# Kernel tuning notes

Measured on AMD Instinct MI355X. Metric: run time of the kernel, lower is better.

## Reference

```python
import jax, jax.numpy as jnp
import numpy as np

B, T, D, K, NF = 4, 1024, 1024, 4, 4
MAXD = 256          # TemporalEncoding max_delta
NC = 32             # ConceptGraph n_concepts
LN_EPS = 1e-5


def setup_inputs() -> dict:
    key = jax.random.key(0)
    ks = jax.random.split(key, 12)
    s = 0.02  # weight init scale
    return {
        "x": jax.random.normal(ks[0], (B, T, D), jnp.float32),
        "routed_tokens": jax.random.normal(ks[1], (B, T, K, D), jnp.float32),
        "sim": jax.random.normal(ks[2], (B, T, K), jnp.float32),
        # per-function logic Linear(3D->D), LayerNorm(D), gate Linear(3D->D)
        "Wl": jax.random.normal(ks[3], (NF, 3 * D, D), jnp.float32) * s,
        "bl": jnp.zeros((NF, D), jnp.float32),
        "ln_g": jnp.ones((NF, D), jnp.float32),
        "ln_b": jnp.zeros((NF, D), jnp.float32),
        "Wg": jax.random.normal(ks[4], (NF, 3 * D, D), jnp.float32) * s,
        "bg": jnp.zeros((NF, D), jnp.float32),
        # fn_selector Linear(D -> NF)
        "Wsel": jax.random.normal(ks[5], (D, NF), jnp.float32) * s,
        "bsel": jnp.zeros((NF,), jnp.float32),
        # temporal embedding table [2*max_delta+1, D]
        "delta_table": jax.random.normal(ks[6], (2 * MAXD + 1, D), jnp.float32) * s,
        # VQ codebook (ConceptGraph.embedding buffer)
        "codebook": jax.random.normal(ks[7], (NC, D), jnp.float32),
        "topk_indices": jax.random.randint(ks[8], (B, T, K), 0, T),
    }


def reference(x, routed_tokens, sim, Wl, bl, ln_g, ln_b, Wg, bg,
              Wsel, bsel, delta_table, codebook, topk_indices):
    Bx, Tx, Dx = x.shape
    Kx = routed_tokens.shape[2]
    N = Bx * Tx

    # temporal encoding: delta = t - topk_index, clamped into table range
    t = jnp.arange(Tx)[None, :, None]
    idx = jnp.clip(t - topk_indices + MAXD, 0, 2 * MAXD)
    de = delta_table[idx].reshape(N, Kx, Dx)            # [N,K,D]

    xf = x.reshape(N, Dx)
    rf = routed_tokens.reshape(N, Kx, Dx)
    sf = sim.reshape(N, Kx)

    tok = jnp.broadcast_to(xf[:, None, :], (N, Kx, Dx))
    comb = jnp.concatenate([tok, rf, de], axis=-1)       # [N,K,3D]

    # all NF reasoning functions at once: logic MLP + GELU + LayerNorm
    h = jnp.einsum('nkc,fcd->fnkd', comb, Wl) + bl[:, None, None, :]
    h = jax.nn.gelu(h, approximate=False)
    mu = jnp.mean(h, axis=-1, keepdims=True)
    var = jnp.var(h, axis=-1, keepdims=True)
    h = (h - mu) / jnp.sqrt(var + LN_EPS)
    h = h * ln_g[:, None, None, :] + ln_b[:, None, None, :]  # [F,N,K,D]

    sw = jax.nn.softmax(sf, axis=-1)                     # [N,K]
    arg = jnp.einsum('nk,fnkd->fnd', sw, h)              # [F,N,D]

    tok_f = jnp.broadcast_to(xf[None], (Wl.shape[0], N, Dx))
    gin = jnp.concatenate([tok_f, arg, arg], axis=-1)    # [F,N,3D]
    gate = jax.nn.sigmoid(jnp.einsum('fnc,fcd->fnd', gin, Wg) + bg[:, None, :])

    fw = jax.nn.softmax(xf @ Wsel + bsel, axis=-1)       # [N,F]
    proposed = jnp.einsum('nf,fnd->nd', fw, arg)
    gsum = jnp.einsum('nf,fnd->nd', fw, gate)
    uf = proposed * gsum                                 # [N,D] updated tokens

    # ConceptGraph VQ (eval: no EMA update): pairwise dist, argmin, gather
    d2 = (jnp.sum(uf * uf, axis=1, keepdims=True)
          - 2.0 * uf @ codebook.T
          + jnp.sum(codebook * codebook, axis=1))        # [N,NC]
    enc = jnp.argmin(d2, axis=1)                         # [N]
    quant = codebook[enc]                                # [N,D]
    out = uf + jax.lax.stop_gradient(quant - uf)         # straight-through
    return out.reshape(Bx, Tx, Dx)
```

## Files before the change

kernel.cpp:

```cpp
#include <hip/hip_runtime.h>
#include <hip/hip_bf16.h>
#include <cmath>


typedef __bf16 bf16x8 __attribute__((ext_vector_type(8)));
typedef float  f32x4  __attribute__((ext_vector_type(4)));

__device__ __forceinline__ float gelu_f(float v) {
    return 0.5f * v * (1.0f + erff(v * 0.7071067811865476f));
}

__device__ __forceinline__ void split8(const float* v, bf16x8& H, bf16x8& L) {
#pragma unroll
    for (int j = 0; j < 8; ++j) {
        float x = v[j];
        __bf16 h = (__bf16)x;
        H[j] = h;
        L[j] = (__bf16)(x - (float)h);
    }
}

#define GLL16(src, dst)                                                        \
    __builtin_amdgcn_global_load_lds(                                          \
        (const __attribute__((address_space(1))) void*)(src),                  \
        (__attribute__((address_space(3))) void*)(dst), 16, 0, 0)

#define SWZ_DECODE()                                                           \
    int bx, by, bz;                                                            \
    {                                                                          \
        const int nx = gridDim.x, ny = gridDim.y;                              \
        const int nwg = nx * ny * (int)gridDim.z;                              \
        const int bid = blockIdx.x + nx * (blockIdx.y + ny * blockIdx.z);      \
        const int q = nwg >> 3;                                                \
        const int rm = (bid & 7) * q + (bid >> 3);                             \
        bx = rm % nx; by = (rm / nx) % ny; bz = rm / (nx * ny);                \
    }

#define WAIT_VM(N)                                                             \
    asm volatile("s_waitcnt vmcnt(" #N ")" ::: "memory");                      \
    __builtin_amdgcn_sched_barrier(0);
#define WAIT_LGKM0()                                                           \
    asm volatile("s_waitcnt lgkmcnt(0)" ::: "memory");                         \
    __builtin_amdgcn_sched_barrier(0);

__global__ __launch_bounds__(256) void precvt_img(
    const float* __restrict__ W, char* __restrict__ img,
    int krowBase, int nktLog, int sumFromKt)
{
    const int u = blockIdx.x * 256 + threadIdx.x;
    const int col = u & 127;
    const int kt  = (u >> 7) & ((1 << nktLog) - 1);
    const int ct  = (u >> (7 + nktLog)) & 7;
    const int f   = u >> (10 + nktLog);
    const int colg = ct * 128 + col;
    const float* Wf = W + (size_t)f * 3072 * 1024;
    const bool sum2 = (kt >= sumFromKt);

    float vv[32];
#pragma unroll
    for (int j = 0; j < 32; ++j) {
        int k = krowBase + kt * 32 + j;
        float v = Wf[(size_t)k * 1024 + colg];
        if (sum2) v += Wf[(size_t)(k + 1024) * 1024 + colg];
        vv[j] = v;
    }
    char* tb = img + ((((size_t)f * 8 + ct) << nktLog) + kt) * 16384;
    const int swz = (col >> 1) & 3;
#pragma unroll
    for (int g = 0; g < 4; ++g) {
        bf16x8 H, L; split8(&vv[g * 8], H, L);
        char* dst = tb + col * 64 + ((g ^ swz) << 4);
        *(bf16x8*)dst = H;
        *(bf16x8*)(dst + 8192) = L;
    }
}

#define WRITEA_SPLIT(AB)                                                       \
    {                                                                          \
        int row = tid >> 2, ag = tid & 3;                                      \
        bf16x8 H, L; split8(ra[0], H, L);                                      \
        char* d = (AB) + row * 64 + ((ag ^ ((row >> 1) & 3)) << 4);            \
        *(bf16x8*)d = H; *(bf16x8*)(d + 8192) = L;                             \
        int row2 = row + 64;                                                   \
        split8(ra[1], H, L);                                                   \
        char* d2 = (AB) + row2 * 64 + ((ag ^ ((row2 >> 1) & 3)) << 4);         \
        *(bf16x8*)d2 = H; *(bf16x8*)(d2 + 8192) = L;                           \
    }

#define LOADB_IMG(KT, BB)                                                      \
    {                                                                          \
        const char* sb = Bt + (size_t)(KT) * 16384 + boff;                     \
        char* db = (BB) + boff;                                                \
        GLL16(sb,        db);                                                  \
        GLL16(sb + 1024, db + 1024);                                           \
        GLL16(sb + 2048, db + 2048);                                           \
        GLL16(sb + 3072, db + 3072);                                           \
    }

#define MFMA32(AB, BB)                                                         \
    {                                                                          \
        bf16x8 ah[4], al[4], bh[4], bl_[4];                                    \
        _Pragma("unroll")                                                      \
        for (int mi = 0; mi < 4; ++mi) {                                       \
            const char* pa = (AB) + (wr + mi * 16 + rl) * 64 + goff;           \
            ah[mi] = *(const bf16x8*)pa;                                       \
            al[mi] = *(const bf16x8*)(pa + 8192);                              \
        }                                                                      \
        _Pragma("unroll")                                                      \
        for (int ni = 0; ni < 4; ++ni) {                                       \
            const char* pb = (BB) + (wc + ni * 16 + rl) * 64 + goff;           \
            bh[ni]  = *(const bf16x8*)pb;                                      \
            bl_[ni] = *(const bf16x8*)(pb + 8192);                             \
        }                                                                      \
        _Pragma("unroll")                                                      \
        for (int mi = 0; mi < 4; ++mi)                                         \
            _Pragma("unroll")                                                  \
            for (int ni = 0; ni < 4; ++ni) {                                   \
                acc[mi][ni] = __builtin_amdgcn_mfma_f32_16x16x32_bf16(ah[mi], bh[ni],  acc[mi][ni], 0, 0, 0); \
                acc[mi][ni] = __builtin_amdgcn_mfma_f32_16x16x32_bf16(ah[mi], bl_[ni], acc[mi][ni], 0, 0, 0); \
                acc[mi][ni] = __builtin_amdgcn_mfma_f32_16x16x32_bf16(al[mi], bh[ni],  acc[mi][ni], 0, 0, 0); \
            }                                                                  \
    }

#define PIPE_LOOP(NKT, LOADA_MACRO)                                            \
    LOADA_MACRO(0)                                                             \
    LOADB_IMG(0, Bc0)                                                          \
    WRITEA_SPLIT(Ac)                                                           \
    LOADA_MACRO(1)                                                             \
    LOADB_IMG(1, Bc1)                                                          \
    WAIT_VM(8)                                                                 \
    WAIT_LGKM0()                                                               \
    __builtin_amdgcn_s_barrier();                                              \
    for (int kt = 0; kt < (NKT); ++kt) {                                       \
        if (kt + 1 < (NKT)) { WRITEA_SPLIT(An) }                               \
        if (kt + 2 < (NKT)) { LOADA_MACRO(kt + 2) LOADB_IMG(kt + 2, Bc2) }     \
        MFMA32(Ac, Bc0)                                                        \
        if (kt + 1 < (NKT)) {                                                  \
            if (kt + 2 < (NKT)) { WAIT_VM(8) } else { WAIT_VM(0) }             \
            WAIT_LGKM0()                                                       \
            __builtin_amdgcn_s_barrier();                                      \
        }                                                                      \
        char* bt = Bc0; Bc0 = Bc1; Bc1 = Bc2; Bc2 = bt;                        \
        char* at = Ac; Ac = An; An = at;                                       \
    }

__global__ __launch_bounds__(256, 2) void gemm_img(
    const float* __restrict__ A, int rowBase,
    const char* __restrict__ img, int fimgBase,
    float* __restrict__ C, size_t cStrideZ)
{
    __shared__ __align__(16) char lds[81920];
    const int tid = threadIdx.x, wid = tid >> 6, lane = tid & 63;
    SWZ_DECODE();
    const int bm0 = bx * 128, bn0 = by * 128;
    const int fimg = fimgBase + bz;
    const char* Bt = img + (size_t)((fimg * 8 + by) << 5) * 16384;
    float* Cp = C + (size_t)bz * cStrideZ;
    const int wr = (wid >> 1) * 64, wc = (wid & 1) * 64;
    const int g = lane >> 4, rl = lane & 15;
    const int goff = ((g ^ ((rl >> 1) & 3)) << 4);
    const int boff = wid * 4096 + lane * 16;
    char* Ac = lds;            char* An = lds + 16384;
    char* Bc0 = lds + 32768;   char* Bc1 = lds + 49152;   char* Bc2 = lds + 65536;

    const float* abase = A + (size_t)(rowBase + bm0 + (tid >> 2)) * 1024 + (tid & 3) * 8;
    float ra[2][8];
#define LOADA_H(KT)                                                            \
    {                                                                          \
        const float* s = abase + (KT) * 32;                                    \
        *(float4*)&ra[0][0] = ((const float4*)s)[0];                           \
        *(float4*)&ra[0][4] = ((const float4*)s)[1];                           \
        const float* s2 = s + 64 * 1024;                                       \
        *(float4*)&ra[1][0] = ((const float4*)s2)[0];                          \
        *(float4*)&ra[1][4] = ((const float4*)s2)[1];                          \
    }

    f32x4 acc[4][4];
    f32x4 zero = {0.f, 0.f, 0.f, 0.f};
#pragma unroll
    for (int i = 0; i < 4; ++i)
#pragma unroll
        for (int j = 0; j < 4; ++j) acc[i][j] = zero;

    PIPE_LOOP(32, LOADA_H)
#undef LOADA_H

    const int cg = lane & 15, rg = (lane >> 4) * 4;
#pragma unroll
    for (int mi = 0; mi < 4; ++mi)
#pragma unroll
        for (int i = 0; i < 4; ++i) {
            int row_out = bm0 + wr + mi * 16 + rg + i;
#pragma unroll
            for (int ni = 0; ni < 4; ++ni) {
                int col = bn0 + wc + ni * 16 + cg;
                Cp[(size_t)row_out * 1024 + col] = acc[mi][ni][i];
            }
        }
}

__global__ __launch_bounds__(256, 2) void gate_img(
    const float* __restrict__ x, const float* __restrict__ arg,
    const char* __restrict__ img, const float* __restrict__ fw,
    const float* __restrict__ bg, float* __restrict__ g2, int fbase)
{
    __shared__ __align__(16) char lds[81920];
    const int tid = threadIdx.x, wid = tid >> 6, lane = tid & 63;
    SWZ_DECODE();
    const int bm0 = bx * 128, bn0 = by * 128;
    const int z = bz, f = fbase + z;
    const float* argf = arg + (size_t)f * 4096 * 1024;
    const char* Bt = img + (size_t)((f * 8 + by) << 6) * 16384;
    const int wr = (wid >> 1) * 64, wc = (wid & 1) * 64;
    const int g = lane >> 4, rl = lane & 15;
    const int goff = ((g ^ ((rl >> 1) & 3)) << 4);
    const int boff = wid * 4096 + lane * 16;
    char* Ac = lds;            char* An = lds + 16384;
    char* Bc0 = lds + 32768;   char* Bc1 = lds + 49152;   char* Bc2 = lds + 65536;

    const int arow = bm0 + (tid >> 2);
    const int akc  = (tid & 3) * 8;
    float ra[2][8];
#define LOADA_G(KT)                                                            \
    {                                                                          \
        int k0 = (KT) * 32 + akc;                                              \
        const float* base = (k0 < 1024) ? x : (argf - 1024);                   \
        const float* s  = base + (size_t)arow * 1024 + k0;                     \
        const float* s2 = base + (size_t)(arow + 64) * 1024 + k0;              \
        *(float4*)&ra[0][0] = ((const float4*)s)[0];                           \
        *(float4*)&ra[0][4] = ((const float4*)s)[1];                           \
        *(float4*)&ra[1][0] = ((const float4*)s2)[0];                          \
        *(float4*)&ra[1][4] = ((const float4*)s2)[1];                          \
    }

    f32x4 acc[4][4];
    f32x4 zero = {0.f, 0.f, 0.f, 0.f};
#pragma unroll
    for (int i = 0; i < 4; ++i)
#pragma unroll
        for (int j = 0; j < 4; ++j) acc[i][j] = zero;

    PIPE_LOOP(64, LOADA_G)
#undef LOADA_G

    const int cg = lane & 15, rg = (lane >> 4) * 4;
    const bool accum = (fbase > 0);
#pragma unroll
    for (int mi = 0; mi < 4; ++mi)
#pragma unroll
        for (int i = 0; i < 4; ++i) {
            int row_out = bm0 + wr + mi * 16 + rg + i;
            float fwv = fw[(size_t)row_out * 4 + f];
#pragma unroll
            for (int ni = 0; ni < 4; ++ni) {
                int col = bn0 + wc + ni * 16 + cg;
                float v = acc[mi][ni][i] + bg[f * 1024 + col];
                float s = fwv / (1.0f + expf(-v));
                size_t off = ((size_t)z * 4096 + row_out) * 1024 + col;
                if (accum) g2[off] += s; else g2[off] = s;
            }
        }
}

#define STAGE_WRITE64()                                                        \
    _Pragma("unroll")                                                          \
    for (int i = 0; i < 4; ++i) {                                              \
        int u = tid + i * 256;                                                 \
        int arow = u >> 3, ag = u & 7;                                         \
        bf16x8 H, L; split8(rav[i], H, L);                                     \
        char* dst = lds + arow * 128 + ((ag ^ (arow & 7)) << 4);               \
        *(bf16x8*)dst = H; *(bf16x8*)(dst + 16384) = L;                        \
    }                                                                          \
    _Pragma("unroll")                                                          \
    for (int i = 0; i < 4; ++i) {                                              \
        int u = tid + i * 256;                                                 \
        int bcol = u & 127, bgu = u >> 7;                                      \
        bf16x8 H, L; split8(rbv[i], H, L);                                     \
        char* dst = lds + 32768 + bcol * 128 + ((bgu ^ (bcol & 7)) << 4);      \
        *(bf16x8*)dst = H; *(bf16x8*)(dst + 16384) = L;                        \
    }

#define MFMA64()                                                               \
    _Pragma("unroll")                                                          \
    for (int ks2 = 0; ks2 < 2; ++ks2) {                                        \
        bf16x8 ah[4], al[4], bh[4], bl_[4];                                    \
        _Pragma("unroll")                                                      \
        for (int mi = 0; mi < 4; ++mi) {                                       \
            const char* pa = lds + (wr + mi * 16 + rl) * 128                   \
                             + (((ks2 * 4 + g) ^ (rl & 7)) << 4);              \
            ah[mi] = *(const bf16x8*)pa;                                       \
            al[mi] = *(const bf16x8*)(pa + 16384);                             \
        }                                                                      \
        _Pragma("unroll")                                                      \
        for (int ni = 0; ni < 4; ++ni) {                                       \
            const char* pb = lds + 32768 + (wc + ni * 16 + rl) * 128           \
                             + (((ks2 * 4 + g) ^ (rl & 7)) << 4);              \
            bh[ni]  = *(const bf16x8*)pb;                                      \
            bl_[ni] = *(const bf16x8*)(pb + 16384);                            \
        }                                                                      \
        _Pragma("unroll")                                                      \
        for (int mi = 0; mi < 4; ++mi)                                         \
            _Pragma("unroll")                                                  \
            for (int ni = 0; ni < 4; ++ni) {                                   \
                acc[mi][ni] = __builtin_amdgcn_mfma_f32_16x16x32_bf16(ah[mi], bh[ni],  acc[mi][ni], 0, 0, 0); \
                acc[mi][ni] = __builtin_amdgcn_mfma_f32_16x16x32_bf16(ah[mi], bl_[ni], acc[mi][ni], 0, 0, 0); \
                acc[mi][ni] = __builtin_amdgcn_mfma_f32_16x16x32_bf16(al[mi], bh[ni],  acc[mi][ni], 0, 0, 0); \
            }                                                                  \
    }

__global__ __launch_bounds__(256, 2) void deproj_part(
    const float* __restrict__ dtab, const float* __restrict__ Wl,
    float* __restrict__ pbase)
{
    __shared__ __align__(16) char lds[65536];
    const int tid = threadIdx.x, wid = tid >> 6, lane = tid & 63;
    SWZ_DECODE();
    const int bm0 = bx * 128, bn0 = by * 128;
    const int f = bz & 3, ks = bz >> 2;
    const int akb = ks * 256;
    const float* Bf = Wl + (size_t)f * 3072 * 1024 + (size_t)(2048 + ks * 256) * 1024;
    float* Cp = pbase + (size_t)ks * 2101248 + (size_t)f * 525312;
    const int wr = (wid >> 1) * 64, wc = (wid & 1) * 64;
    const int g = lane >> 4, rl = lane & 15;

    float rav[4][8], rbv[4][8];

#define LOADA_D(KC0)                                                           \
    _Pragma("unroll")                                                          \
    for (int i = 0; i < 4; ++i) {                                              \
        int u = tid + i * 256;                                                 \
        int r = bm0 + (u >> 3); if (r > 512) r = 512;                          \
        const float* s = dtab + (size_t)r * 1024 + akb + (KC0) + (u & 7) * 8;  \
        *(float4*)&rav[i][0] = ((const float4*)s)[0];                          \
        *(float4*)&rav[i][4] = ((const float4*)s)[1];                          \
    }
#define LOADB_D(KC0)                                                           \
    _Pragma("unroll")                                                          \
    for (int i = 0; i < 4; ++i) {                                              \
        int u = tid + i * 256;                                                 \
        int bcol = bn0 + (u & 127);                                            \
        int k0 = (KC0) + (u >> 7) * 8;                                         \
        _Pragma("unroll")                                                      \
        for (int j = 0; j < 8; ++j)                                            \
            rbv[i][j] = Bf[(size_t)(k0 + j) * 1024 + bcol];                    \
    }

    f32x4 acc[4][4];
    f32x4 zero = {0.f, 0.f, 0.f, 0.f};
#pragma unroll
    for (int i = 0; i < 4; ++i)
#pragma unroll
        for (int j = 0; j < 4; ++j) acc[i][j] = zero;

    LOADA_D(0) LOADB_D(0)
    for (int kt = 0; kt < 4; ++kt) {
        STAGE_WRITE64()
        __syncthreads();
        if (kt + 1 < 4) { LOADA_D((kt + 1) * 64) LOADB_D((kt + 1) * 64) }
        MFMA64()
        __syncthreads();
    }
#undef LOADA_D
#undef LOADB_D

    const int cg = lane & 15, rg = (lane >> 4) * 4;
#pragma unroll
    for (int mi = 0; mi < 4; ++mi)
#pragma unroll
        for (int i = 0; i < 4; ++i) {
            int row_out = bm0 + wr + mi * 16 + rg + i;
            if (row_out >= 513) continue;
#pragma unroll
            for (int ni = 0; ni < 4; ++ni) {
                int col = bn0 + wc + ni * 16 + cg;
                Cp[(size_t)row_out * 1024 + col] = acc[mi][ni][i];
            }
        }
}

__global__ __launch_bounds__(256) void deproj_reduce(float* __restrict__ p)
{
    const size_t i = ((size_t)blockIdx.x * 256 + threadIdx.x) * 4;
    float4 a = *(float4*)&p[i];
    float4 b = *(const float4*)&p[i + 2101248];
    float4 c = *(const float4*)&p[i + 4202496];
    float4 d = *(const float4*)&p[i + 6303744];
    a.x = ((a.x + b.x) + c.x) + d.x;
    a.y = ((a.y + b.y) + c.y) + d.y;
    a.z = ((a.z + b.z) + c.z) + d.z;
    a.w = ((a.w + b.w) + c.w) + d.w;
    *(float4*)&p[i] = a;
}

__global__ __launch_bounds__(256) void fw_kernel(
    const float* __restrict__ x, const float* __restrict__ Wsel,
    const float* __restrict__ bsel, float* __restrict__ fw)
{
    __shared__ float sred[16];
    const int n = blockIdx.x;
    const int tid = threadIdx.x, w = tid >> 6, lane = tid & 63;

    float4 xv = *(const float4*)&x[(size_t)n * 1024 + tid * 4];
    float pf0 = 0, pf1 = 0, pf2 = 0, pf3 = 0;
    const float* wrp = &Wsel[(size_t)tid * 16];
    pf0 += xv.x * wrp[0];  pf1 += xv.x * wrp[1];  pf2 += xv.x * wrp[2];  pf3 += xv.x * wrp[3];
    pf0 += xv.y * wrp[4];  pf1 += xv.y * wrp[5];  pf2 += xv.y * wrp[6];  pf3 += xv.y * wrp[7];
    pf0 += xv.z * wrp[8];  pf1 += xv.z * wrp[9];  pf2 += xv.z * wrp[10]; pf3 += xv.z * wrp[11];
    pf0 += xv.w * wrp[12]; pf1 += xv.w * wrp[13]; pf2 += xv.w * wrp[14]; pf3 += xv.w * wrp[15];
    for (int o = 32; o; o >>= 1) {
        pf0 += __shfl_xor(pf0, o); pf1 += __shfl_xor(pf1, o);
        pf2 += __shfl_xor(pf2, o); pf3 += __shfl_xor(pf3, o);
    }
    if (lane == 0) { sred[w*4+0] = pf0; sred[w*4+1] = pf1; sred[w*4+2] = pf2; sred[w*4+3] = pf3; }
    __syncthreads();
    if (tid == 0) {
        float s0 = sred[0] + sred[4] + sred[8]  + sred[12] + bsel[0];
        float s1 = sred[1] + sred[5] + sred[9]  + sred[13] + bsel[1];
        float s2 = sred[2] + sred[6] + sred[10] + sred[14] + bsel[2];
        float s3 = sred[3] + sred[7] + sred[11] + sred[15] + bsel[3];
        float mx = fmaxf(fmaxf(s0, s1), fmaxf(s2, s3));
        float e0 = expf(s0 - mx), e1 = expf(s1 - mx), e2 = expf(s2 - mx), e3 = expf(s3 - mx);
        float inv = 1.0f / (e0 + e1 + e2 + e3);
        float4 o = { e0 * inv, e1 * inv, e2 * inv, e3 * inv };
        *(float4*)&fw[(size_t)n * 4] = o;
    }
}

__global__ __launch_bounds__(256) void ln_fuse_kernel(
    const float* __restrict__ hpre, const float* __restrict__ de_proj,
    const float* __restrict__ bl, const float* __restrict__ ln_g,
    const float* __restrict__ ln_b, const float* __restrict__ sim,
    const int* __restrict__ topk, float* arg,
    int f, int token_base, const float* xl)
{
    __shared__ float red[4 * 1024];
    const int n = token_base + blockIdx.x;
    const int k = threadIdx.x >> 6, lane = threadIdx.x & 63;
    const float* hrow = hpre + ((size_t)blockIdx.x * 4 + k) * 1024;
    const int t  = n & 1023;
    const int tk = topk[(size_t)n * 4 + k];
    int di = t - tk + 256; di = di < 0 ? 0 : (di > 512 ? 512 : di);
    const float* drow = de_proj + ((size_t)f * 513 + di) * 1024;
    const float* blr = bl + f * 1024;
    const float* gr  = ln_g + f * 1024;
    const float* br  = ln_b + f * 1024;
    const float* xr  = xl + (size_t)n * 1024;

    float4 s4 = *(const float4*)&sim[(size_t)n * 4];
    float smax = fmaxf(fmaxf(s4.x, s4.y), fmaxf(s4.z, s4.w));
    float e0 = expf(s4.x - smax), e1 = expf(s4.y - smax);
    float e2 = expf(s4.z - smax), e3 = expf(s4.w - smax);
    float swk = (k == 0 ? e0 : k == 1 ? e1 : k == 2 ? e2 : e3) / (e0 + e1 + e2 + e3);

    float gv[16];
    float ssum = 0.f;
#pragma unroll
    for (int j = 0; j < 4; ++j) {
        int d4 = lane + j * 64;
        float4 h  = *(const float4*)&hrow[d4 * 4];
        float4 dd = *(const float4*)&drow[d4 * 4];
        float4 bb = *(const float4*)&blr[d4 * 4];
        float4 xv = *(const float4*)&xr[d4 * 4];
        float a0 = gelu_f(h.x + xv.x + dd.x + bb.x);
        float a1 = gelu_f(h.y + xv.y + dd.y + bb.y);
        float a2 = gelu_f(h.z + xv.z + dd.z + bb.z);
        float a3 = gelu_f(h.w + xv.w + dd.w + bb.w);
        gv[j*4+0] = a0; gv[j*4+1] = a1; gv[j*4+2] = a2; gv[j*4+3] = a3;
        ssum += a0 + a1 + a2 + a3;
    }
    for (int o = 32; o; o >>= 1) ssum += __shfl_xor(ssum, o);
    float mu = ssum * 0.0009765625f;
    float vs = 0.f;
#pragma unroll
    for (int i = 0; i < 16; ++i) { float dm = gv[i] - mu; vs += dm * dm; }
    for (int o = 32; o; o >>= 1) vs += __shfl_xor(vs, o);
    float rstd = 1.0f / sqrtf(vs * 0.0009765625f + 1e-5f);
#pragma unroll
    for (int j = 0; j < 4; ++j) {
        int d4 = lane + j * 64;
        float4 g4 = *(const float4*)&gr[d4 * 4];
        float4 b4 = *(const float4*)&br[d4 * 4];
        float4 y;
        y.x = ((gv[j*4+0] - mu) * rstd * g4.x + b4.x) * swk;
        y.y = ((gv[j*4+1] - mu) * rstd * g4.y + b4.y) * swk;
        y.z = ((gv[j*4+2] - mu) * rstd * g4.z + b4.z) * swk;
        y.w = ((gv[j*4+3] - mu) * rstd * g4.w + b4.w) * swk;
        *(float4*)&red[k * 1024 + d4 * 4] = y;
    }
    __syncthreads();
    const int p = threadIdx.x;
    float4 r0 = *(const float4*)&red[0 * 1024 + p * 4];
    float4 r1 = *(const float4*)&red[1 * 1024 + p * 4];
    float4 r2 = *(const float4*)&red[2 * 1024 + p * 4];
    float4 r3 = *(const float4*)&red[3 * 1024 + p * 4];
    float4 o;
    o.x = r0.x + r1.x + r2.x + r3.x;
    o.y = r0.y + r1.y + r2.y + r3.y;
    o.z = r0.z + r1.z + r2.z + r3.z;
    o.w = r0.w + r1.w + r2.w + r3.w;
    *(float4*)&arg[((size_t)f * 4096 + n) * 1024 + p * 4] = o;
}

__global__ __launch_bounds__(256) void final_kernel(
    const float* __restrict__ fw, const float* __restrict__ arg,
    const float* __restrict__ g2, const float* __restrict__ cb,
    float* __restrict__ out)
{
    __shared__ float uf_s[1024];
    __shared__ float score_s[32];
    __shared__ int enc_s;
    const int n = blockIdx.x;
    const int tid = threadIdx.x, w = tid >> 6, lane = tid & 63;

    float4 fwv = *(const float4*)&fw[(size_t)n * 4];
    float fwa[4] = { fwv.x, fwv.y, fwv.z, fwv.w };

    float4 prop = {0, 0, 0, 0};
#pragma unroll
    for (int f = 0; f < 4; ++f) {
        float4 av = *(const float4*)&arg[((size_t)f * 4096 + n) * 1024 + tid * 4];
        prop.x += fwa[f] * av.x; prop.y += fwa[f] * av.y;
        prop.z += fwa[f] * av.z; prop.w += fwa[f] * av.w;
    }
    float4 ga = *(const float4*)&g2[(size_t)n * 1024 + tid * 4];
    float4 gb = *(const float4*)&g2[(size_t)(4096 + n) * 1024 + tid * 4];
    float4 uf;
    uf.x = prop.x * (ga.x + gb.x); uf.y = prop.y * (ga.y + gb.y);
    uf.z = prop.z * (ga.z + gb.z); uf.w = prop.w * (ga.w + gb.w);
    *(float4*)&uf_s[tid * 4] = uf;
    __syncthreads();

#pragma unroll
    for (int cc = 0; cc < 8; ++cc) {
        int c = w * 8 + cc;
        float p = 0.f, q = 0.f;
#pragma unroll
        for (int j = 0; j < 4; ++j) {
            int d4 = lane + j * 64;
            float4 u4 = *(const float4*)&uf_s[d4 * 4];
            float4 c4 = *(const float4*)&cb[(size_t)c * 1024 + d4 * 4];
            p += u4.x * c4.x + u4.y * c4.y + u4.z * c4.z + u4.w * c4.w;
            q += c4.x * c4.x + c4.y * c4.y + c4.z * c4.z + c4.w * c4.w;
        }
        float s = q - 2.0f * p;
        for (int o = 32; o; o >>= 1) s += __shfl_xor(s, o);
        if (lane == 0) score_s[c] = s;
    }
    __syncthreads();
    if (tid < 64) {
        float v; int idx;
        if (lane < 32) { v = score_s[lane]; idx = lane; }
        else           { v = INFINITY;      idx = 1 << 30; }
        for (int o = 16; o; o >>= 1) {
            float ov = __shfl_xor(v, o); int oi = __shfl_xor(idx, o);
            if (ov < v || (ov == v && oi < idx)) { v = ov; idx = oi; }
        }
        if (lane == 0) enc_s = idx;
    }
    __syncthreads();
    const int enc = enc_s;
    float4 o4 = *(const float4*)&cb[(size_t)enc * 1024 + tid * 4];
    *(float4*)&out[(size_t)n * 1024 + tid * 4] = o4;
}

extern "C" void kernel_launch(void* const* d_in, const int* in_sizes, int n_in,
                              void* d_out, int out_size, void* d_ws, size_t ws_size,
                              hipStream_t stream)
{
    const float* x    = (const float*)d_in[0];
    const float* rf   = (const float*)d_in[1];
    const float* sim  = (const float*)d_in[2];
    const float* Wl   = (const float*)d_in[3];
    const float* bl   = (const float*)d_in[4];
    const float* ln_g = (const float*)d_in[5];
    const float* ln_b = (const float*)d_in[6];
    const float* Wg   = (const float*)d_in[7];
    const float* bg   = (const float*)d_in[8];
    const float* Wsel = (const float*)d_in[9];
    const float* bsel = (const float*)d_in[10];
    const float* dtab = (const float*)d_in[11];
    const float* cb   = (const float*)d_in[12];
    const int*   topk = (const int*)d_in[13];
    float* out = (float*)d_out;
    dim3 blk(256);

    const size_t NEED = 142622720ull;
    if (ws_size < NEED) return;
    char* ws = (char*)d_ws;
    float* arg     = (float*)(ws + 0);
    float* de_proj = (float*)(ws + 67108864);
    float* hbuf    = (float*)(ws + 75513856);
    char*  Wl1img  = ws + 109068288;
    char*  Wl0img  = ws + 125845504;
    char*  Wgimg   = ws + 67108864;
    float* g2      = (float*)(ws + 100663296);
    float* fw      = (float*)(ws + 134217728);

    deproj_part<<<dim3(5, 8, 16), blk, 0, stream>>>(dtab, Wl, de_proj);
    deproj_reduce<<<2052, blk, 0, stream>>>(de_proj);

    precvt_img<<<512, blk, 0, stream>>>(Wl, Wl0img, 0, 5, 99);
    gemm_img<<<dim3(32, 8, 4), blk, 0, stream>>>(
        x, 0, Wl0img, 0, arg, (size_t)4096 * 1024);

    precvt_img<<<512, blk, 0, stream>>>(Wl, Wl1img, 1024, 5, 99);

    for (int f = 0; f < 4; ++f) {
        const float* xlf = arg + (size_t)f * 4096 * 1024;
        for (int ch = 0; ch < 2; ++ch) {
            gemm_img<<<dim3(64, 8, 1), blk, 0, stream>>>(
                rf, ch * 8192, Wl1img, f, hbuf, 0);
            ln_fuse_kernel<<<2048, blk, 0, stream>>>(
                hbuf, de_proj, bl, ln_g, ln_b, sim, topk, arg,
                f, ch * 2048, xlf);
        }
    }

    precvt_img<<<1024, blk, 0, stream>>>(Wg, Wgimg, 0, 6, 32);

    fw_kernel<<<4096, blk, 0, stream>>>(x, Wsel, bsel, fw);

    gate_img<<<dim3(32, 8, 2), blk, 0, stream>>>(x, arg, Wgimg, fw, bg, g2, 0);
    gate_img<<<dim3(32, 8, 2), blk, 0, stream>>>(x, arg, Wgimg, fw, bg, g2, 2);

    final_kernel<<<4096, blk, 0, stream>>>(fw, arg, g2, cb, out);
}
```

Before: 948.9 us.

## Load A fragments straight into registers, bypassing LDS, and raise occupancy

The A operand of the split-bf16 GEMMs was staged through LDS. Now each wave loads its own rows of fp32 A from global memory directly into registers and splits them into hi/lo bf16 in registers. This drops the LDS A buffers and their waits, shrinking LDS from 80KB to 48KB, and launch bounds are raised to 3 blocks per CU. The cost is that A is read redundantly by the two column waves, with more global loads and register pressure, which could cause spills at the higher occupancy target.

```diff
diff --git a/kernel.cpp b/kernel.cpp
--- a/kernel.cpp
+++ b/kernel.cpp
@@ -39,9 +39,6 @@
 #define WAIT_VM(N)                                                             \
     asm volatile("s_waitcnt vmcnt(" #N ")" ::: "memory");                      \
     __builtin_amdgcn_sched_barrier(0);
-#define WAIT_LGKM0()                                                           \
-    asm volatile("s_waitcnt lgkmcnt(0)" ::: "memory");                         \
-    __builtin_amdgcn_sched_barrier(0);
 
 __global__ __launch_bounds__(256) void precvt_img(
     const float* __restrict__ W, char* __restrict__ img,
@@ -75,18 +72,6 @@
     }
 }
 
-#define WRITEA_SPLIT(AB)                                                       \
-    {                                                                          \
-        int row = tid >> 2, ag = tid & 3;                                      \
-        bf16x8 H, L; split8(ra[0], H, L);                                      \
-        char* d = (AB) + row * 64 + ((ag ^ ((row >> 1) & 3)) << 4);            \
-        *(bf16x8*)d = H; *(bf16x8*)(d + 8192) = L;                             \
-        int row2 = row + 64;                                                   \
-        split8(ra[1], H, L);                                                   \
-        char* d2 = (AB) + row2 * 64 + ((ag ^ ((row2 >> 1) & 3)) << 4);         \
-        *(bf16x8*)d2 = H; *(bf16x8*)(d2 + 8192) = L;                           \
-    }
-
 #define LOADB_IMG(KT, BB)                                                      \
     {                                                                          \
         const char* sb = Bt + (size_t)(KT) * 16384 + boff;                     \
@@ -97,15 +82,13 @@
         GLL16(sb + 3072, db + 3072);                                           \
     }
 
-#define MFMA32(AB, BB)                                                         \
+#define SPLIT4()                                                               \
+    _Pragma("unroll")                                                          \
+    for (int mi = 0; mi < 4; ++mi) split8(araw[mi], ahC[mi], alC[mi]);
+
+#define MFMA32REG(BB)                                                          \
     {                                                                          \
-        bf16x8 ah[4], al[4], bh[4], bl_[4];                                    \
-        _Pragma("unroll")                                                      \
-        for (int mi = 0; mi < 4; ++mi) {                                       \
-            const char* pa = (AB) + (wr + mi * 16 + rl) * 64 + goff;           \
-            ah[mi] = *(const bf16x8*)pa;                                       \
-            al[mi] = *(const bf16x8*)(pa + 8192);                              \
-        }                                                                      \
+        bf16x8 bh[4], bl_[4];                                                  \
         _Pragma("unroll")                                                      \
         for (int ni = 0; ni < 4; ++ni) {                                       \
             const char* pb = (BB) + (wc + ni * 16 + rl) * 64 + goff;           \
@@ -116,40 +99,38 @@
         for (int mi = 0; mi < 4; ++mi)                                         \
             _Pragma("unroll")                                                  \
             for (int ni = 0; ni < 4; ++ni) {                                   \
-                acc[mi][ni] = __builtin_amdgcn_mfma_f32_16x16x32_bf16(ah[mi], bh[ni],  acc[mi][ni], 0, 0, 0); \
-                acc[mi][ni] = __builtin_amdgcn_mfma_f32_16x16x32_bf16(ah[mi], bl_[ni], acc[mi][ni], 0, 0, 0); \
-                acc[mi][ni] = __builtin_amdgcn_mfma_f32_16x16x32_bf16(al[mi], bh[ni],  acc[mi][ni], 0, 0, 0); \
+                acc[mi][ni] = __builtin_amdgcn_mfma_f32_16x16x32_bf16(ahC[mi], bh[ni],  acc[mi][ni], 0, 0, 0); \
+                acc[mi][ni] = __builtin_amdgcn_mfma_f32_16x16x32_bf16(ahC[mi], bl_[ni], acc[mi][ni], 0, 0, 0); \
+                acc[mi][ni] = __builtin_amdgcn_mfma_f32_16x16x32_bf16(alC[mi], bh[ni],  acc[mi][ni], 0, 0, 0); \
             }                                                                  \
     }
 
-#define PIPE_LOOP(NKT, LOADA_MACRO)                                            \
+#define PIPE_LOOP_R(NKT, LOADA_MACRO)                                          \
     LOADA_MACRO(0)                                                             \
     LOADB_IMG(0, Bc0)                                                          \
-    WRITEA_SPLIT(Ac)                                                           \
+    LOADB_IMG(1, Bc1)                                                          \
+    WAIT_VM(4)                                                                 \
+    SPLIT4()                                                                   \
     LOADA_MACRO(1)                                                             \
-    LOADB_IMG(1, Bc1)                                                          \
-    WAIT_VM(8)                                                                 \
-    WAIT_LGKM0()                                                               \
     __builtin_amdgcn_s_barrier();                                              \
     for (int kt = 0; kt < (NKT); ++kt) {                                       \
-        if (kt + 1 < (NKT)) { WRITEA_SPLIT(An) }                               \
-        if (kt + 2 < (NKT)) { LOADA_MACRO(kt + 2) LOADB_IMG(kt + 2, Bc2) }     \
-        MFMA32(Ac, Bc0)                                                        \
+        if (kt + 2 < (NKT)) { LOADB_IMG(kt + 2, Bc2) }                         \
+        MFMA32REG(Bc0)                                                         \
         if (kt + 1 < (NKT)) {                                                  \
-            if (kt + 2 < (NKT)) { WAIT_VM(8) } else { WAIT_VM(0) }             \
-            WAIT_LGKM0()                                                       \
+            if (kt + 2 < (NKT)) { WAIT_VM(4) } else { WAIT_VM(0) }             \
+            SPLIT4()                                                           \
+            if (kt + 2 < (NKT)) { LOADA_MACRO(kt + 2) }                        \
             __builtin_amdgcn_s_barrier();                                      \
         }                                                                      \
         char* bt = Bc0; Bc0 = Bc1; Bc1 = Bc2; Bc2 = bt;                        \
-        char* at = Ac; Ac = An; An = at;                                       \
-    }
-
-__global__ __launch_bounds__(256, 2) void gemm_img(
+    }
+
+__global__ __launch_bounds__(256, 3) void gemm_img(
     const float* __restrict__ A, int rowBase,
     const char* __restrict__ img, int fimgBase,
     float* __restrict__ C, size_t cStrideZ)
 {
-    __shared__ __align__(16) char lds[81920];
+    __shared__ __align__(16) char lds[49152];
     const int tid = threadIdx.x, wid = tid >> 6, lane = tid & 63;
     SWZ_DECODE();
     const int bm0 = bx * 128, bn0 = by * 128;
@@ -160,19 +141,20 @@
     const int g = lane >> 4, rl = lane & 15;
     const int goff = ((g ^ ((rl >> 1) & 3)) << 4);
     const int boff = wid * 4096 + lane * 16;
-    char* Ac = lds;            char* An = lds + 16384;
-    char* Bc0 = lds + 32768;   char* Bc1 = lds + 49152;   char* Bc2 = lds + 65536;
-
-    const float* abase = A + (size_t)(rowBase + bm0 + (tid >> 2)) * 1024 + (tid & 3) * 8;
-    float ra[2][8];
-#define LOADA_H(KT)                                                            \
+    char* Bc0 = lds; char* Bc1 = lds + 16384; char* Bc2 = lds + 32768;
+
+    const float* aBase = A + (size_t)(rowBase + bm0 + wr + rl) * 1024 + g * 8;
+    float araw[4][8];
+    bf16x8 ahC[4], alC[4];
+#define LOADA_R(KT)                                                            \
     {                                                                          \
-        const float* s = abase + (KT) * 32;                                    \
-        *(float4*)&ra[0][0] = ((const float4*)s)[0];                           \
-        *(float4*)&ra[0][4] = ((const float4*)s)[1];                           \
-        const float* s2 = s + 64 * 1024;                                       \
-        *(float4*)&ra[1][0] = ((const float4*)s2)[0];                          \
-        *(float4*)&ra[1][4] = ((const float4*)s2)[1];                          \
+        const float* s0 = aBase + (KT) * 32;                                   \
+        _Pragma("unroll")                                                      \
+        for (int mi = 0; mi < 4; ++mi) {                                       \
+            const float* s = s0 + mi * 16384;                                  \
+            *(float4*)&araw[mi][0] = ((const float4*)s)[0];                    \
+            *(float4*)&araw[mi][4] = ((const float4*)s)[1];                    \
+        }                                                                      \
     }
 
     f32x4 acc[4][4];
@@ -182,8 +164,8 @@
 #pragma unroll
         for (int j = 0; j < 4; ++j) acc[i][j] = zero;
 
-    PIPE_LOOP(32, LOADA_H)
-#undef LOADA_H
+    PIPE_LOOP_R(32, LOADA_R)
+#undef LOADA_R
 
     const int cg = lane & 15, rg = (lane >> 4) * 4;
 #pragma unroll
@@ -199,12 +181,12 @@
         }
 }
 
-__global__ __launch_bounds__(256, 2) void gate_img(
+__global__ __launch_bounds__(256, 3) void gate_img(
     const float* __restrict__ x, const float* __restrict__ arg,
     const char* __restrict__ img, const float* __restrict__ fw,
     const float* __restrict__ bg, float* __restrict__ g2, int fbase)
 {
-    __shared__ __align__(16) char lds[81920];
+    __shared__ __align__(16) char lds[49152];
     const int tid = threadIdx.x, wid = tid >> 6, lane = tid & 63;
     SWZ_DECODE();
     const int bm0 = bx * 128, bn0 = by * 128;
@@ -215,22 +197,23 @@
     const int g = lane >> 4, rl = lane & 15;
     const int goff = ((g ^ ((rl >> 1) & 3)) << 4);
     const int boff = wid * 4096 + lane * 16;
-    char* Ac = lds;            char* An = lds + 16384;
-    char* Bc0 = lds + 32768;   char* Bc1 = lds + 49152;   char* Bc2 = lds + 65536;
-
-    const int arow = bm0 + (tid >> 2);
-    const int akc  = (tid & 3) * 8;
-    float ra[2][8];
+    char* Bc0 = lds; char* Bc1 = lds + 16384; char* Bc2 = lds + 32768;
+
+    const size_t rowoff = (size_t)(bm0 + wr + rl) * 1024 + g * 8;
+    const float* xab = x + rowoff;
+    const float* aab = argf + rowoff - 1024;
+    float araw[4][8];
+    bf16x8 ahC[4], alC[4];
 #define LOADA_G(KT)                                                            \
     {                                                                          \
-        int k0 = (KT) * 32 + akc;                                              \
-        const float* base = (k0 < 1024) ? x : (argf - 1024);                   \
-        const float* s  = base + (size_t)arow * 1024 + k0;                     \
-        const float* s2 = base + (size_t)(arow + 64) * 1024 + k0;              \
-        *(float4*)&ra[0][0] = ((const float4*)s)[0];                           \
-        *(float4*)&ra[0][4] = ((const float4*)s)[1];                           \
-        *(float4*)&ra[1][0] = ((const float4*)s2)[0];                          \
-        *(float4*)&ra[1][4] = ((const float4*)s2)[1];                          \
+        const int k0g = (KT) * 32;                                             \
+        const float* s0 = (k0g < 1024 ? xab : aab) + k0g;                      \
+        _Pragma("unroll")                                                      \
+        for (int mi = 0; mi < 4; ++mi) {                                       \
+            const float* s = s0 + mi * 16384;                                  \
+            *(float4*)&araw[mi][0] = ((const float4*)s)[0];                    \
+            *(float4*)&araw[mi][4] = ((const float4*)s)[1];                    \
+        }                                                                      \
     }
 
     f32x4 acc[4][4];
@@ -240,7 +223,7 @@
 #pragma unroll
         for (int j = 0; j < 4; ++j) acc[i][j] = zero;
 
-    PIPE_LOOP(64, LOADA_G)
+    PIPE_LOOP_R(64, LOADA_G)
 #undef LOADA_G
 
     const int cg = lane & 15, rg = (lane >> 4) * 4;
```

New measurement: 1.327 ms. +39.8%, slower.

## Pre-split A operands into bf16 hi/lo images and reorder loops to reuse them

Applied to the files above, without the earlier changes.

Adds a precvt_a kernel that converts fp32 activations (x and routed tokens) once into swizzled bf16 hi/lo tile images. A new gemm_ii kernel then streams both A and B with direct global-to-LDS loads, with no per-tile register split. The loop over routed chunks now converts each 4096-row chunk once and reuses it across all four functions, where previously the fp32 split was redone for every function. This costs an extra pass writing and reading the A images and reuses workspace regions, and it depends on ln_fuse handling the new chunking correctly.

```diff
diff --git a/kernel.cpp b/kernel.cpp
--- a/kernel.cpp
+++ b/kernel.cpp
@@ -75,27 +75,30 @@
     }
 }
 
-#define WRITEA_SPLIT(AB)                                                       \
-    {                                                                          \
-        int row = tid >> 2, ag = tid & 3;                                      \
-        bf16x8 H, L; split8(ra[0], H, L);                                      \
-        char* d = (AB) + row * 64 + ((ag ^ ((row >> 1) & 3)) << 4);            \
-        *(bf16x8*)d = H; *(bf16x8*)(d + 8192) = L;                             \
-        int row2 = row + 64;                                                   \
-        split8(ra[1], H, L);                                                   \
-        char* d2 = (AB) + row2 * 64 + ((ag ^ ((row2 >> 1) & 3)) << 4);         \
-        *(bf16x8*)d2 = H; *(bf16x8*)(d2 + 8192) = L;                           \
-    }
-
-#define LOADB_IMG(KT, BB)                                                      \
-    {                                                                          \
-        const char* sb = Bt + (size_t)(KT) * 16384 + boff;                     \
-        char* db = (BB) + boff;                                                \
-        GLL16(sb,        db);                                                  \
-        GLL16(sb + 1024, db + 1024);                                           \
-        GLL16(sb + 2048, db + 2048);                                           \
-        GLL16(sb + 3072, db + 3072);                                           \
-    }
+__global__ __launch_bounds__(256) void precvt_a(
+    const float* __restrict__ src, int rowBase, char* __restrict__ img)
+{
+    const int u = blockIdx.x * 256 + threadIdx.x;
+    const int row = u & 127;
+    const int kt  = (u >> 7) & 31;
+    const int rt  = u >> 12;
+    const float* s = src + (size_t)(rowBase + rt * 128 + row) * 1024 + kt * 32;
+    float vv[32];
+#pragma unroll
+    for (int j = 0; j < 8; ++j) {
+        float4 v4 = ((const float4*)s)[j];
+        vv[j*4+0] = v4.x; vv[j*4+1] = v4.y; vv[j*4+2] = v4.z; vv[j*4+3] = v4.w;
+    }
+    char* tb = img + (size_t)(rt * 32 + kt) * 16384;
+    const int swz = (row >> 1) & 3;
+#pragma unroll
+    for (int g = 0; g < 4; ++g) {
+        bf16x8 H, L; split8(&vv[g * 8], H, L);
+        char* dst = tb + row * 64 + ((g ^ swz) << 4);
+        *(bf16x8*)dst = H;
+        *(bf16x8*)(dst + 8192) = L;
+    }
+}
 
 #define MFMA32(AB, BB)                                                         \
     {                                                                          \
@@ -122,6 +125,95 @@
             }                                                                  \
     }
 
+__global__ __launch_bounds__(256, 2) void gemm_ii(
+    const char* __restrict__ Aimg, const char* __restrict__ Bimg,
+    int fimgBase, float* __restrict__ C, size_t cStrideZ)
+{
+    __shared__ __align__(16) char lds[81920];
+    const int tid = threadIdx.x, wid = tid >> 6, lane = tid & 63;
+    SWZ_DECODE();
+    const int bm0 = bx * 128, bn0 = by * 128;
+    const char* At = Aimg + (size_t)(bx << 5) * 16384;
+    const char* Bt = Bimg + (size_t)(((fimgBase + bz) * 8 + by) << 5) * 16384;
+    float* Cp = C + (size_t)bz * cStrideZ;
+    const int wr = (wid >> 1) * 64, wc = (wid & 1) * 64;
+    const int g = lane >> 4, rl = lane & 15;
+    const int goff = ((g ^ ((rl >> 1) & 3)) << 4);
+    const int boff = wid * 4096 + lane * 16;
+    char* Ac = lds;            char* An = lds + 16384;
+    char* Bc0 = lds + 32768;   char* Bc1 = lds + 49152;   char* Bc2 = lds + 65536;
+
+#define GLLT(TB, KT, BB)                                                       \
+    {                                                                          \
+        const char* sb = (TB) + (size_t)(KT) * 16384 + boff;                   \
+        char* db = (BB) + boff;                                                \
+        GLL16(sb,        db);                                                  \
+        GLL16(sb + 1024, db + 1024);                                           \
+        GLL16(sb + 2048, db + 2048);                                           \
+        GLL16(sb + 3072, db + 3072);                                           \
+    }
+
+    f32x4 acc[4][4];
+    f32x4 zero = {0.f, 0.f, 0.f, 0.f};
+#pragma unroll
+    for (int i = 0; i < 4; ++i)
+#pragma unroll
+        for (int j = 0; j < 4; ++j) acc[i][j] = zero;
+
+    GLLT(Bt, 0, Bc0)
+    GLLT(At, 0, Ac)
+    GLLT(Bt, 1, Bc1)
+    WAIT_VM(4)
+    __builtin_amdgcn_s_barrier();
+    for (int kt = 0; kt < 32; ++kt) {
+        if (kt + 1 < 32) { GLLT(At, kt + 1, An) }
+        if (kt + 2 < 32) { GLLT(Bt, kt + 2, Bc2) }
+        MFMA32(Ac, Bc0)
+        if (kt + 1 < 32) {
+            if (kt + 2 < 32) { WAIT_VM(4) } else { WAIT_VM(0) }
+            __builtin_amdgcn_s_barrier();
+        }
+        char* at = Ac; Ac = An; An = at;
+        char* bt2 = Bc0; Bc0 = Bc1; Bc1 = Bc2; Bc2 = bt2;
+    }
+#undef GLLT
+
+    const int cg = lane & 15, rg = (lane >> 4) * 4;
+#pragma unroll
+    for (int mi = 0; mi < 4; ++mi)
+#pragma unroll
+        for (int i = 0; i < 4; ++i) {
+            int row_out = bm0 + wr + mi * 16 + rg + i;
+#pragma unroll
+            for (int ni = 0; ni < 4; ++ni) {
+                int col = bn0 + wc + ni * 16 + cg;
+                Cp[(size_t)row_out * 1024 + col] = acc[mi][ni][i];
+            }
+        }
+}
+
+#define WRITEA_SPLIT(AB)                                                       \
+    {                                                                          \
+        int row = tid >> 2, ag = tid & 3;                                      \
+        bf16x8 H, L; split8(ra[0], H, L);                                      \
+        char* d = (AB) + row * 64 + ((ag ^ ((row >> 1) & 3)) << 4);            \
+        *(bf16x8*)d = H; *(bf16x8*)(d + 8192) = L;                             \
+        int row2 = row + 64;                                                   \
+        split8(ra[1], H, L);                                                   \
+        char* d2 = (AB) + row2 * 64 + ((ag ^ ((row2 >> 1) & 3)) << 4);         \
+        *(bf16x8*)d2 = H; *(bf16x8*)(d2 + 8192) = L;                           \
+    }
+
+#define LOADB_IMG(KT, BB)                                                      \
+    {                                                                          \
+        const char* sb = Bt + (size_t)(KT) * 16384 + boff;                     \
+        char* db = (BB) + boff;                                                \
+        GLL16(sb,        db);                                                  \
+        GLL16(sb + 1024, db + 1024);                                           \
+        GLL16(sb + 2048, db + 2048);                                           \
+        GLL16(sb + 3072, db + 3072);                                           \
+    }
+
 #define PIPE_LOOP(NKT, LOADA_MACRO)                                            \
     LOADA_MACRO(0)                                                             \
     LOADB_IMG(0, Bc0)                                                          \
@@ -143,61 +235,6 @@
         char* bt = Bc0; Bc0 = Bc1; Bc1 = Bc2; Bc2 = bt;                        \
         char* at = Ac; Ac = An; An = at;                                       \
     }
-
-__global__ __launch_bounds__(256, 2) void gemm_img(
-    const float* __restrict__ A, int rowBase,
-    const char* __restrict__ img, int fimgBase,
-    float* __restrict__ C, size_t cStrideZ)
-{
-    __shared__ __align__(16) char lds[81920];
-    const int tid = threadIdx.x, wid = tid >> 6, lane = tid & 63;
-    SWZ_DECODE();
-    const int bm0 = bx * 128, bn0 = by * 128;
-    const int fimg = fimgBase + bz;
-    const char* Bt = img + (size_t)((fimg * 8 + by) << 5) * 16384;
-    float* Cp = C + (size_t)bz * cStrideZ;
-    const int wr = (wid >> 1) * 64, wc = (wid & 1) * 64;
-    const int g = lane >> 4, rl = lane & 15;
-    const int goff = ((g ^ ((rl >> 1) & 3)) << 4);
-    const int boff = wid * 4096 + lane * 16;
-    char* Ac = lds;            char* An = lds + 16384;
-    char* Bc0 = lds + 32768;   char* Bc1 = lds + 49152;   char* Bc2 = lds + 65536;
-
-    const float* abase = A + (size_t)(rowBase + bm0 + (tid >> 2)) * 1024 + (tid & 3) * 8;
-    float ra[2][8];
-#define LOADA_H(KT)                                                            \
-    {                                                                          \
-        const float* s = abase + (KT) * 32;                                    \
-        *(float4*)&ra[0][0] = ((const float4*)s)[0];                           \
-        *(float4*)&ra[0][4] = ((const float4*)s)[1];                           \
-        const float* s2 = s + 64 * 1024;                                       \
-        *(float4*)&ra[1][0] = ((const float4*)s2)[0];                          \
-        *(float4*)&ra[1][4] = ((const float4*)s2)[1];                          \
-    }
-
-    f32x4 acc[4][4];
-    f32x4 zero = {0.f, 0.f, 0.f, 0.f};
-#pragma unroll
-    for (int i = 0; i < 4; ++i)
-#pragma unroll
-        for (int j = 0; j < 4; ++j) acc[i][j] = zero;
-
-    PIPE_LOOP(32, LOADA_H)
-#undef LOADA_H
-
-    const int cg = lane & 15, rg = (lane >> 4) * 4;
-#pragma unroll
-    for (int mi = 0; mi < 4; ++mi)
-#pragma unroll
-        for (int i = 0; i < 4; ++i) {
-            int row_out = bm0 + wr + mi * 16 + rg + i;
-#pragma unroll
-            for (int ni = 0; ni < 4; ++ni) {
-                int col = bn0 + wc + ni * 16 + cg;
-                Cp[(size_t)row_out * 1024 + col] = acc[mi][ni][i];
-            }
-        }
-}
 
 __global__ __launch_bounds__(256, 2) void gate_img(
     const float* __restrict__ x, const float* __restrict__ arg,
@@ -590,8 +627,10 @@
     float* arg     = (float*)(ws + 0);
     float* de_proj = (float*)(ws + 67108864);
     float* hbuf    = (float*)(ws + 75513856);
+    char*  ximg    = ws + 75513856;
     char*  Wl1img  = ws + 109068288;
     char*  Wl0img  = ws + 125845504;
+    char*  rfimg   = ws + 125845504;
     char*  Wgimg   = ws + 67108864;
     float* g2      = (float*)(ws + 100663296);
     float* fw      = (float*)(ws + 134217728);
@@ -599,20 +638,25 @@
     deproj_part<<<dim3(5, 8, 16), blk, 0, stream>>>(dtab, Wl, de_proj);
     deproj_reduce<<<2052, blk, 0, stream>>>(de_proj);
 
+    precvt_a<<<512, blk, 0, stream>>>(x, 0, ximg);
     precvt_img<<<512, blk, 0, stream>>>(Wl, Wl0img, 0, 5, 99);
-    gemm_img<<<dim3(32, 8, 4), blk, 0, stream>>>(
-        x, 0, Wl0img, 0, arg, (size_t)4096 * 1024);
+    gemm_ii<<<dim3(32, 8, 4), blk, 0, stream>>>(
+        ximg, Wl0img, 0, arg, (size_t)4096 * 1024);
 
     precvt_img<<<512, blk, 0, stream>>>(Wl, Wl1img, 1024, 5, 99);
 
-    for (int f = 0; f < 4; ++f) {
-        const float* xlf = arg + (size_t)f * 4096 * 1024;
-        for (int ch = 0; ch < 2; ++ch) {
-            gemm_img<<<dim3(64, 8, 1), blk, 0, stream>>>(
-                rf, ch * 8192, Wl1img, f, hbuf, 0);
-            ln_fuse_kernel<<<2048, blk, 0, stream>>>(
-                hbuf, de_proj, bl, ln_g, ln_b, sim, topk, arg,
-                f, ch * 2048, xlf);
+    for (int ch = 0; ch < 4; ++ch) {
+        precvt_a<<<512, blk, 0, stream>>>(rf, ch * 4096, rfimg);
+        for (int fp = 0; fp < 2; ++fp) {
+            gemm_ii<<<dim3(32, 8, 2), blk, 0, stream>>>(
+                rfimg, Wl1img, fp * 2, hbuf, (size_t)4096 * 1024);
+            for (int zi = 0; zi < 2; ++zi) {
+                int f = fp * 2 + zi;
+                ln_fuse_kernel<<<1024, blk, 0, stream>>>(
+                    hbuf + (size_t)zi * 4194304, de_proj, bl, ln_g, ln_b,
+                    sim, topk, arg, f, ch * 1024,
+                    arg + (size_t)f * 4194304);
+            }
         }
     }
 
```

Measured after the change: 987.9 us. +4.1%, slower.
